# Optimization experiments

Measured on AMD Instinct MI355X. Metric: run time of the kernel, lower is better.

The kernel has to match this reference:

```python
import jax, jax.numpy as jnp
import numpy as np

N = 100_000   # nodes
E = 3_200_000 # edges (avg degree 32)
IN = 256      # input feature dim


def setup_inputs() -> dict:
    key = jax.random.key(0)
    ks = jax.random.split(key, 10)
    w = lambda k, s: (jax.random.normal(k, s, jnp.float32) * 0.02)
    return {
        "x": jax.random.normal(ks[0], (N, IN), jnp.float32),
        "edge_index": jax.random.randint(ks[1], (2, E), 0, N, dtype=jnp.int32),
        "edge_attr": jax.random.normal(ks[2], (E, 1), jnp.float32),
        # conv1: ExpGraphConv(IN, 64, 128)
        "W1a": w(ks[3], (IN, 64)), "b1a": jnp.zeros((64,), jnp.float32),
        "W1b": w(ks[4], (IN + 64, 128)), "b1b": jnp.zeros((128,), jnp.float32),
        # conv2: ExpGraphConv(128, 32->hidden 64? per ctor (128, 32, 64)): msg hidden 32... kept as repo: hidden=32? Using (128,64) msg, (192,64) out per faithful cat structure
        "W2a": w(ks[5], (128, 64)), "b2a": jnp.zeros((64,), jnp.float32),
        "W2b": w(ks[6], (128 + 64, 64)), "b2b": jnp.zeros((64,), jnp.float32),
        # head
        "Wl1": w(ks[7], (64, 32)), "bl1": jnp.zeros((32,), jnp.float32),
        "Wl2": w(ks[8], (32, 1)), "bl2": jnp.zeros((1,), jnp.float32),
    }


def _mean_aggr(h, src, dst, n):
    # gather messages from source nodes, scatter-mean into destination nodes
    s = jax.ops.segment_sum(h[src], dst, num_segments=n)          # [N, d]
    cnt = jax.ops.segment_sum(jnp.ones((src.shape[0],), h.dtype), dst, num_segments=n)
    return s / jnp.maximum(cnt, 1.0)[:, None]


def _exp_graph_conv(x, src, dst, Wa, ba, Wb, bb):
    # message MLP on source features, mean aggregation, then linear on [x || aggr]
    h = x @ Wa + ba                                               # [N, hidden]
    m = _mean_aggr(h, src, dst, x.shape[0])                       # [N, hidden]
    return jnp.concatenate([x, m], axis=1) @ Wb + bb              # [N, out]


def reference(x, edge_index, edge_attr, W1a, b1a, W1b, b1b, W2a, b2a, W2b, b2b, Wl1, bl1, Wl2, bl2):
    src, dst = edge_index[0], edge_index[1]
    x = jax.nn.relu(_exp_graph_conv(x, src, dst, W1a, b1a, W1b, b1b))
    x = jax.nn.relu(_exp_graph_conv(x, src, dst, W2a, b2a, W2b, b2b))
    x = jax.nn.relu(x @ Wl1 + bl1)
    return x @ Wl2 + bl2
```

## Files before the change

kernel.cpp:

```cpp
#include <hip/hip_runtime.h>
#include <type_traits>

#define IN_DIM 256
#define CAP 10240
#define EPB 4096

typedef _Float16 f16;
typedef _Float16 f16x8 __attribute__((ext_vector_type(8)));
typedef float f32x4 __attribute__((ext_vector_type(4)));


__global__ __launch_bounds__(256) void init_cur_k(int* __restrict__ bcur) {
    int i = blockIdx.x * 256 + threadIdx.x;
    if (i < 512) bcur[i] = i * CAP;
}

__global__ __launch_bounds__(256) void bucket_scatter_k(const int* __restrict__ srcp,
                                                        const int* __restrict__ dstp,
                                                        int* __restrict__ bcur,
                                                        unsigned* __restrict__ bedge, int E) {
    __shared__ int cnt[512], lstart[512], delta[512], fill[512];
    __shared__ int pfx[256];
    __shared__ unsigned spay[EPB];
    __shared__ unsigned char sbk[EPB];
    int tid = threadIdx.x;
    cnt[tid] = 0; cnt[tid + 256] = 0;
    fill[tid] = 0; fill[tid + 256] = 0;
    __syncthreads();
    size_t base = (size_t)blockIdx.x * EPB;
    int nloc = E - (int)base; if (nloc > EPB) nloc = EPB;
    int dreg[EPB / 256], sreg[EPB / 256];
#pragma unroll
    for (int j = 0; j < EPB / 256; j++) {
        int e = j * 256 + tid;
        if (e < nloc) {
            dreg[j] = dstp[base + e];
            sreg[j] = srcp[base + e];
            atomicAdd(&cnt[dreg[j] >> 8], 1);
        }
    }
    __syncthreads();
    int a0 = cnt[2 * tid], a1 = cnt[2 * tid + 1], s = a0 + a1;
    pfx[tid] = s;
    __syncthreads();
    for (int off = 1; off < 256; off <<= 1) {
        int t2 = (tid >= off) ? pfx[tid - off] : 0;
        __syncthreads();
        pfx[tid] += t2;
        __syncthreads();
    }
    int excl = pfx[tid] - s;
    lstart[2 * tid] = excl;
    lstart[2 * tid + 1] = excl + a0;
    int g0 = 0, g1 = 0;
    if (a0) g0 = atomicAdd(&bcur[2 * tid], a0);
    if (a1) g1 = atomicAdd(&bcur[2 * tid + 1], a1);
    delta[2 * tid] = g0 - excl;
    delta[2 * tid + 1] = g1 - (excl + a0);
    __syncthreads();
#pragma unroll
    for (int j = 0; j < EPB / 256; j++) {
        int e = j * 256 + tid;
        if (e < nloc) {
            int d = dreg[j], bk = d >> 8;
            int slot = lstart[bk] + atomicAdd(&fill[bk], 1);
            spay[slot] = (unsigned)sreg[j] | ((unsigned)(d & 255) << 17);
            sbk[slot] = (unsigned char)bk;
        }
    }
    __syncthreads();
    int mid = lstart[256];
#pragma unroll
    for (int j = 0; j < EPB / 256; j++) {
        int i = j * 256 + tid;
        if (i < nloc) {
            int bk = (int)sbk[i] | ((i >= mid) ? 256 : 0);
            int gp = i + delta[bk];
            if (gp < (bk + 1) * CAP)
                bedge[gp] = spay[i];
        }
    }
}

__global__ __launch_bounds__(256) void fine_sort_k(unsigned* __restrict__ bedge,
                                                   const int* __restrict__ bcur,
                                                   int2* __restrict__ ose, int Nn) {
    __shared__ int cnt[256], cur[256], pfx[256];
    __shared__ int sorted[CAP];
    int b = blockIdx.x, tid = threadIdx.x;
    int lo = b * CAP;
    int sz = bcur[b] - lo;
    if (sz > CAP) sz = CAP;
    cnt[tid] = 0;
    __syncthreads();
    for (int i = tid; i < sz; i += 256) atomicAdd(&cnt[bedge[lo + i] >> 17], 1);
    __syncthreads();
    int c = cnt[tid];
    pfx[tid] = c;
    __syncthreads();
    for (int off = 1; off < 256; off <<= 1) {
        int t2 = (tid >= off) ? pfx[tid - off] : 0;
        __syncthreads();
        pfx[tid] += t2;
        __syncthreads();
    }
    int excl = pfx[tid] - c;
    cur[tid] = excl;
    int node = b * 256 + tid;
    if (node < Nn) ose[node] = make_int2(lo + excl, lo + excl + c);
    __syncthreads();
    for (int i = tid; i < sz; i += 256) {
        unsigned v = bedge[lo + i];
        int slot = atomicAdd(&cur[v >> 17], 1);
        sorted[slot] = (int)(v & 0x1FFFFu);
    }
    __syncthreads();
    for (int i = tid; i < sz; i += 256) bedge[lo + i] = (unsigned)sorted[i];
}


__global__ __launch_bounds__(256) void castf16_k(const float* __restrict__ X,
                                                 f16* __restrict__ Y, int n4) {
    int i = blockIdx.x * 256 + threadIdx.x;
    if (i >= n4) return;
    float4 v = reinterpret_cast<const float4*>(X)[i];
    union { f16 h[4]; uint2 u; } p;
    p.h[0] = (f16)v.x; p.h[1] = (f16)v.y; p.h[2] = (f16)v.z; p.h[3] = (f16)v.w;
    reinterpret_cast<uint2*>(Y)[i] = p.u;
}

__global__ __launch_bounds__(256) void wcast_k(const float* __restrict__ W,
                                               f16* __restrict__ Wt, int K, int N) {
    int i = blockIdx.x * 256 + threadIdx.x;
    if (i >= N * K) return;
    int n = i / K, k = i - n * K;
    Wt[i] = (f16)W[(size_t)k * N + n];
}


__global__ __launch_bounds__(256) void aggr_k(const int2* __restrict__ ose,
                                              const int* __restrict__ ssrc,
                                              const f16* __restrict__ h,
                                              f16* __restrict__ m, int n) {
    int wave = (blockIdx.x * 256 + threadIdx.x) >> 6;
    int lane = threadIdx.x & 63;
    if (wave >= n) return;
    int2 se = ose[wave];
    int s0 = se.x, s1 = se.y;
    int half = lane >> 5;
    int l32 = lane & 31;
    const unsigned* h32 = reinterpret_cast<const unsigned*>(h);
    float ax = 0.f, ay = 0.f;
    for (int c = s0; c < s1; c += 64) {
        int cn = min(64, s1 - c);
        int myidx = (lane < cn) ? ssrc[c + lane] : 0;
        int t = 0;
        for (; t + 8 <= cn; t += 8) {
            int ia = __shfl(myidx, t + 0 + half);
            int ib = __shfl(myidx, t + 2 + half);
            int ic = __shfl(myidx, t + 4 + half);
            int id = __shfl(myidx, t + 6 + half);
            unsigned ua = h32[(size_t)ia * 32 + l32];
            unsigned ub = h32[(size_t)ib * 32 + l32];
            unsigned uc = h32[(size_t)ic * 32 + l32];
            unsigned ud = h32[(size_t)id * 32 + l32];
            union { unsigned u; f16 hh[2]; } qa, qb, qc, qd;
            qa.u = ua; qb.u = ub; qc.u = uc; qd.u = ud;
            ax += (float)qa.hh[0] + (float)qb.hh[0] + (float)qc.hh[0] + (float)qd.hh[0];
            ay += (float)qa.hh[1] + (float)qb.hh[1] + (float)qc.hh[1] + (float)qd.hh[1];
        }
        for (; t + 2 <= cn; t += 2) {
            int ia = __shfl(myidx, t + half);
            unsigned ua = h32[(size_t)ia * 32 + l32];
            union { unsigned u; f16 hh[2]; } qa; qa.u = ua;
            ax += (float)qa.hh[0];
            ay += (float)qa.hh[1];
        }
        if (t < cn) {
            int ia = __shfl(myidx, t);
            if (half == 0) {
                unsigned ua = h32[(size_t)ia * 32 + l32];
                union { unsigned u; f16 hh[2]; } qa; qa.u = ua;
                ax += (float)qa.hh[0];
                ay += (float)qa.hh[1];
            }
        }
    }
    ax += __shfl_xor(ax, 32);
    ay += __shfl_xor(ay, 32);
    if (half == 0) {
        float inv = 1.0f / fmaxf((float)(s1 - s0), 1.0f);
        union { unsigned u; f16 hh[2]; } q;
        q.hh[0] = (f16)(ax * inv);
        q.hh[1] = (f16)(ay * inv);
        reinterpret_cast<unsigned*>(m + (size_t)wave * 64)[l32] = q.u;
    }
}


template <int BN, bool OUT_F16>
__global__ __launch_bounds__(256) void gemm_mfma(const f16* __restrict__ A1, int K1,
                                                 const f16* __restrict__ A2, int K2,
                                                 const f16* __restrict__ Wt,
                                                 const float* __restrict__ bias,
                                                 void* __restrict__ Yv, int M, int relu) {
    constexpr int BM = 128, BK = 32;
    constexpr int WN = BN / 2;
    constexpr int NB = WN / 16;
    constexpr int SEGB = BN / 64;
    using T = typename std::conditional<OUT_F16, f16, float>::type;
    constexpr int EPS = BN + 8;
    constexpr int VECN = 16 / sizeof(T);
    constexpr int TPR = BN / VECN;
    constexpr size_t SM_AB = (size_t)BM * BK * 2 + (size_t)BN * BK * 2;
    constexpr size_t SM_EP = (size_t)BM * EPS * sizeof(T);
    constexpr size_t SM = SM_AB > SM_EP ? SM_AB : SM_EP;
    __shared__ __align__(16) char smem[SM];
    f16 (*As)[BK] = reinterpret_cast<f16(*)[BK]>(smem);
    f16 (*Bs)[BK] = reinterpret_cast<f16(*)[BK]>(smem + (size_t)BM * BK * 2);
    const int tid  = threadIdx.x;
    const int wave = tid >> 6;
    const int lane = tid & 63;
    const int wr   = wave >> 1;
    const int wc   = wave & 1;
    const int quad = lane >> 4;
    const int l16  = lane & 15;
    const int row0 = blockIdx.x * BM;
    const int Ktot = K1 + K2;

    f32x4 acc[4][NB];
#pragma unroll
    for (int i = 0; i < 4; i++)
#pragma unroll
        for (int j = 0; j < NB; j++) acc[i][j] = (f32x4)(0.f);

    const int ra = tid >> 2, sa = tid & 3;
    int rowA0 = row0 + ra;       if (rowA0 >= M) rowA0 = M - 1;
    int rowA1 = row0 + ra + 64;  if (rowA1 >= M) rowA1 = M - 1;

    uint4 aReg[2], bReg[SEGB];
    auto loadA = [&](int kk) {
        const f16* base; int stride, kloc;
        if (kk < K1) { base = A1; stride = K1; kloc = kk; }
        else         { base = A2; stride = K2; kloc = kk - K1; }
        aReg[0] = *reinterpret_cast<const uint4*>(base + (size_t)rowA0 * stride + kloc + sa * 8);
        aReg[1] = *reinterpret_cast<const uint4*>(base + (size_t)rowA1 * stride + kloc + sa * 8);
    };
    auto loadB = [&](int kk) {
#pragma unroll
        for (int i = 0; i < SEGB; i++) {
            int fid = tid + i * 256;
            int n = fid >> 2, s = fid & 3;
            bReg[i] = *reinterpret_cast<const uint4*>(Wt + (size_t)n * Ktot + kk + s * 8);
        }
    };

    loadA(0); loadB(0);
    for (int kk = 0; kk < Ktot; kk += BK) {
        reinterpret_cast<uint4*>(&As[0][0])[tid]       = aReg[0];
        reinterpret_cast<uint4*>(&As[0][0])[tid + 256] = aReg[1];
#pragma unroll
        for (int i = 0; i < SEGB; i++)
            reinterpret_cast<uint4*>(&Bs[0][0])[tid + i * 256] = bReg[i];
        __syncthreads();
        if (kk + BK < Ktot) { loadA(kk + BK); loadB(kk + BK); }
        f16x8 af[4], bf[NB];
#pragma unroll
        for (int rb = 0; rb < 4; rb++) {
            int row = wr * 64 + rb * 16 + l16;
            af[rb] = *reinterpret_cast<const f16x8*>(&As[row][quad * 8]);
        }
#pragma unroll
        for (int cb = 0; cb < NB; cb++) {
            int n = wc * WN + cb * 16 + l16;
            bf[cb] = *reinterpret_cast<const f16x8*>(&Bs[n][quad * 8]);
        }
#pragma unroll
        for (int rb = 0; rb < 4; rb++)
#pragma unroll
            for (int cb = 0; cb < NB; cb++)
                acc[rb][cb] = __builtin_amdgcn_mfma_f32_16x16x32_f16(af[rb], bf[cb], acc[rb][cb], 0, 0, 0);
        __syncthreads();
    }

    T* ep = reinterpret_cast<T*>(smem);
#pragma unroll
    for (int rb = 0; rb < 4; rb++) {
#pragma unroll
        for (int cb = 0; cb < NB; cb++) {
            int col = wc * WN + cb * 16 + l16;
            float bv = bias[col];
#pragma unroll
            for (int r = 0; r < 4; r++) {
                int lrow = wr * 64 + rb * 16 + quad * 4 + r;
                float v = acc[rb][cb][r] + bv;
                if (relu) v = fmaxf(v, 0.f);
                ep[(size_t)lrow * EPS + col] = (T)v;
            }
        }
    }
    __syncthreads();
#pragma unroll
    for (int p = 0; p < BM * TPR / 256; p++) {
        int fid = p * 256 + tid;
        int row = fid / TPR, c = fid % TPR;
        int grow = row0 + row;
        if (grow < M)
            *reinterpret_cast<uint4*>((T*)Yv + (size_t)grow * BN + c * VECN) =
                *reinterpret_cast<const uint4*>(ep + (size_t)row * EPS + c * VECN);
    }
}


__global__ __launch_bounds__(256) void head_k(const float* __restrict__ x2,
                                              const float* __restrict__ Wl1,
                                              const float* __restrict__ bl1,
                                              const float* __restrict__ Wl2,
                                              const float* __restrict__ bl2,
                                              float* __restrict__ out, int n) {
    __shared__ __align__(16) float w1[64 * 32];
    __shared__ float b1s[32];
    __shared__ float w2s[32];
    for (int t = threadIdx.x; t < 2048; t += 256) w1[t] = Wl1[t];
    if (threadIdx.x < 32) {
        b1s[threadIdx.x] = bl1[threadIdx.x];
        w2s[threadIdx.x] = Wl2[threadIdx.x];
    }
    __syncthreads();
    int i = blockIdx.x * 256 + threadIdx.x;
    if (i >= n) return;
    float v[64];
#pragma unroll
    for (int t = 0; t < 16; t++) {
        float4 q = *reinterpret_cast<const float4*>(x2 + (size_t)i * 64 + t * 4);
        v[t * 4 + 0] = q.x; v[t * 4 + 1] = q.y; v[t * 4 + 2] = q.z; v[t * 4 + 3] = q.w;
    }
    float hj[32];
#pragma unroll
    for (int j = 0; j < 32; j++) hj[j] = b1s[j];
    for (int k = 0; k < 64; k++) {
        float vk = v[k];
        const float4* wrow = reinterpret_cast<const float4*>(&w1[k * 32]);
#pragma unroll
        for (int j4 = 0; j4 < 8; j4++) {
            float4 wq = wrow[j4];
            hj[j4 * 4 + 0] += vk * wq.x;
            hj[j4 * 4 + 1] += vk * wq.y;
            hj[j4 * 4 + 2] += vk * wq.z;
            hj[j4 * 4 + 3] += vk * wq.w;
        }
    }
    float o = bl2[0];
#pragma unroll
    for (int j = 0; j < 32; j++) o += fmaxf(hj[j], 0.f) * w2s[j];
    out[i] = o;
}


extern "C" void kernel_launch(void* const* d_in, const int* in_sizes, int n_in,
                              void* d_out, int out_size, void* d_ws, size_t ws_size,
                              hipStream_t stream) {
    const float* x   = (const float*)d_in[0];
    const int*   ei  = (const int*)d_in[1];
    const float* W1a = (const float*)d_in[3];
    const float* b1a = (const float*)d_in[4];
    const float* W1b = (const float*)d_in[5];
    const float* b1b = (const float*)d_in[6];
    const float* W2a = (const float*)d_in[7];
    const float* b2a = (const float*)d_in[8];
    const float* W2b = (const float*)d_in[9];
    const float* b2b = (const float*)d_in[10];
    const float* Wl1 = (const float*)d_in[11];
    const float* bl1 = (const float*)d_in[12];
    const float* Wl2 = (const float*)d_in[13];
    const float* bl2 = (const float*)d_in[14];

    const int N = in_sizes[0] / IN_DIM;
    const int E = in_sizes[1] / 2;
    const int* srcp = ei;
    const int* dstp = ei + E;

    char* ws = (char*)d_ws;
    size_t off = 0;
    auto alloc = [&](size_t bytes) -> char* {
        char* p = ws + off;
        off = (off + bytes + 255) & ~(size_t)255;
        return p;
    };
    int NB2 = (N + 255) / 256;
    int*      bcur  = (int*)alloc(512 * 4);
    unsigned* bedge = (unsigned*)alloc((size_t)NB2 * CAP * 4);
    int2*     ose   = (int2*)alloc((size_t)N * 8);
    f16*      x16   = (f16*)alloc((size_t)N * IN_DIM * 2);
    f16*      hbuf  = (f16*)alloc((size_t)N * 64 * 2);
    f16*      mbuf  = (f16*)alloc((size_t)N * 64 * 2);
    f16*      x1    = (f16*)alloc((size_t)N * 128 * 2);
    float*    h2    = (float*)alloc((size_t)N * 64 * 4);
    f16*      Wt1a  = (f16*)alloc(256 * 64 * 2);
    f16*      Wt1b  = (f16*)alloc(320 * 128 * 2);
    f16*      Wt2a  = (f16*)alloc(128 * 64 * 2);
    f16*      Wt2b  = (f16*)alloc(192 * 64 * 2);
    (void)ws_size;

    init_cur_k<<<2, 256, 0, stream>>>(bcur);
    int ebk = (E + EPB - 1) / EPB;
    bucket_scatter_k<<<ebk, 256, 0, stream>>>(srcp, dstp, bcur, bedge, E);
    fine_sort_k<<<NB2, 256, 0, stream>>>(bedge, bcur, ose, N);

    int n4 = N * IN_DIM / 4;
    castf16_k<<<(n4 + 255) / 256, 256, 0, stream>>>(x, x16, n4);
    wcast_k<<<(256 * 64 + 255) / 256, 256, 0, stream>>>(W1a, Wt1a, 256, 64);
    wcast_k<<<(320 * 128 + 255) / 256, 256, 0, stream>>>(W1b, Wt1b, 320, 128);
    wcast_k<<<(128 * 64 + 255) / 256, 256, 0, stream>>>(W2a, Wt2a, 128, 64);
    wcast_k<<<(192 * 64 + 255) / 256, 256, 0, stream>>>(W2b, Wt2b, 192, 64);

    int mb = (N + 127) / 128;
    int ab = (N * 64 + 255) / 256;

    gemm_mfma<64, true><<<mb, 256, 0, stream>>>(x16, IN_DIM, nullptr, 0, Wt1a, b1a, hbuf, N, 0);
    aggr_k<<<ab, 256, 0, stream>>>(ose, (const int*)bedge, hbuf, mbuf, N);
    gemm_mfma<128, true><<<mb, 256, 0, stream>>>(x16, IN_DIM, mbuf, 64, Wt1b, b1b, x1, N, 1);

    gemm_mfma<64, true><<<mb, 256, 0, stream>>>(x1, 128, nullptr, 0, Wt2a, b2a, hbuf, N, 0);
    aggr_k<<<ab, 256, 0, stream>>>(ose, (const int*)bedge, hbuf, mbuf, N);
    gemm_mfma<64, false><<<mb, 256, 0, stream>>>(x1, 128, mbuf, 64, Wt2b, b2b, h2, N, 1);

    head_k<<<(N + 255) / 256, 256, 0, stream>>>(h2, Wl1, bl1, Wl2, bl2, (float*)d_out, N);
}
```

Baseline: 515.2 us.

## Halve GEMM row tile, add nontemporal loads/stores, store h2 as f16

The GEMM row tile drops from 128 to 64, which launches twice as many blocks with fewer accumulators each. The cast kernel and the GEMM A-operand loads and selected outputs now use nontemporal loads and stores to reduce cache pollution. The layer-2 output h2 is stored as f16 rather than fp32 and read as f16 in the head, halving that traffic at some precision cost. Smaller tiles mean more weight (B) reloads per row processed.

```diff
diff --git a/kernel.cpp b/kernel.cpp
--- a/kernel.cpp
+++ b/kernel.cpp
@@ -8,6 +8,8 @@
 typedef _Float16 f16;
 typedef _Float16 f16x8 __attribute__((ext_vector_type(8)));
 typedef float f32x4 __attribute__((ext_vector_type(4)));
+typedef unsigned u32x4 __attribute__((ext_vector_type(4)));
+typedef unsigned u32x2 __attribute__((ext_vector_type(2)));
 
 
 __global__ __launch_bounds__(256) void init_cur_k(int* __restrict__ bcur) {
@@ -123,10 +125,10 @@
                                                  f16* __restrict__ Y, int n4) {
     int i = blockIdx.x * 256 + threadIdx.x;
     if (i >= n4) return;
-    float4 v = reinterpret_cast<const float4*>(X)[i];
-    union { f16 h[4]; uint2 u; } p;
+    f32x4 v = __builtin_nontemporal_load(reinterpret_cast<const f32x4*>(X) + i);
+    union { f16 h[4]; u32x2 u; } p;
     p.h[0] = (f16)v.x; p.h[1] = (f16)v.y; p.h[2] = (f16)v.z; p.h[3] = (f16)v.w;
-    reinterpret_cast<uint2*>(Y)[i] = p.u;
+    __builtin_nontemporal_store(p.u, reinterpret_cast<u32x2*>(Y) + i);
 }
 
 __global__ __launch_bounds__(256) void wcast_k(const float* __restrict__ W,
@@ -203,8 +205,9 @@
                                                  const f16* __restrict__ A2, int K2,
                                                  const f16* __restrict__ Wt,
                                                  const float* __restrict__ bias,
-                                                 void* __restrict__ Yv, int M, int relu) {
-    constexpr int BM = 128, BK = 32;
+                                                 void* __restrict__ Yv, int M, int relu,
+                                                 int stream_out) {
+    constexpr int BM = 64, BK = 32;
     constexpr int WN = BN / 2;
     constexpr int NB = WN / 16;
     constexpr int SEGB = BN / 64;
@@ -228,46 +231,44 @@
     const int row0 = blockIdx.x * BM;
     const int Ktot = K1 + K2;
 
-    f32x4 acc[4][NB];
-#pragma unroll
-    for (int i = 0; i < 4; i++)
+    f32x4 acc[2][NB];
+#pragma unroll
+    for (int i = 0; i < 2; i++)
 #pragma unroll
         for (int j = 0; j < NB; j++) acc[i][j] = (f32x4)(0.f);
 
     const int ra = tid >> 2, sa = tid & 3;
-    int rowA0 = row0 + ra;       if (rowA0 >= M) rowA0 = M - 1;
-    int rowA1 = row0 + ra + 64;  if (rowA1 >= M) rowA1 = M - 1;
-
-    uint4 aReg[2], bReg[SEGB];
+    int rowA = row0 + ra;  if (rowA >= M) rowA = M - 1;
+
+    u32x4 aReg, bReg[SEGB];
     auto loadA = [&](int kk) {
         const f16* base; int stride, kloc;
         if (kk < K1) { base = A1; stride = K1; kloc = kk; }
         else         { base = A2; stride = K2; kloc = kk - K1; }
-        aReg[0] = *reinterpret_cast<const uint4*>(base + (size_t)rowA0 * stride + kloc + sa * 8);
-        aReg[1] = *reinterpret_cast<const uint4*>(base + (size_t)rowA1 * stride + kloc + sa * 8);
+        aReg = __builtin_nontemporal_load(
+            reinterpret_cast<const u32x4*>(base + (size_t)rowA * stride + kloc + sa * 8));
     };
     auto loadB = [&](int kk) {
 #pragma unroll
         for (int i = 0; i < SEGB; i++) {
             int fid = tid + i * 256;
             int n = fid >> 2, s = fid & 3;
-            bReg[i] = *reinterpret_cast<const uint4*>(Wt + (size_t)n * Ktot + kk + s * 8);
+            bReg[i] = *reinterpret_cast<const u32x4*>(Wt + (size_t)n * Ktot + kk + s * 8);
         }
     };
 
     loadA(0); loadB(0);
     for (int kk = 0; kk < Ktot; kk += BK) {
-        reinterpret_cast<uint4*>(&As[0][0])[tid]       = aReg[0];
-        reinterpret_cast<uint4*>(&As[0][0])[tid + 256] = aReg[1];
+        reinterpret_cast<u32x4*>(&As[0][0])[tid] = aReg;
 #pragma unroll
         for (int i = 0; i < SEGB; i++)
-            reinterpret_cast<uint4*>(&Bs[0][0])[tid + i * 256] = bReg[i];
+            reinterpret_cast<u32x4*>(&Bs[0][0])[tid + i * 256] = bReg[i];
         __syncthreads();
         if (kk + BK < Ktot) { loadA(kk + BK); loadB(kk + BK); }
-        f16x8 af[4], bf[NB];
-#pragma unroll
-        for (int rb = 0; rb < 4; rb++) {
-            int row = wr * 64 + rb * 16 + l16;
+        f16x8 af[2], bf[NB];
+#pragma unroll
+        for (int rb = 0; rb < 2; rb++) {
+            int row = wr * 32 + rb * 16 + l16;
             af[rb] = *reinterpret_cast<const f16x8*>(&As[row][quad * 8]);
         }
 #pragma unroll
@@ -276,7 +277,7 @@
             bf[cb] = *reinterpret_cast<const f16x8*>(&Bs[n][quad * 8]);
         }
 #pragma unroll
-        for (int rb = 0; rb < 4; rb++)
+        for (int rb = 0; rb < 2; rb++)
 #pragma unroll
             for (int cb = 0; cb < NB; cb++)
                 acc[rb][cb] = __builtin_amdgcn_mfma_f32_16x16x32_f16(af[rb], bf[cb], acc[rb][cb], 0, 0, 0);
@@ -285,14 +286,14 @@
 
     T* ep = reinterpret_cast<T*>(smem);
 #pragma unroll
-    for (int rb = 0; rb < 4; rb++) {
+    for (int rb = 0; rb < 2; rb++) {
 #pragma unroll
         for (int cb = 0; cb < NB; cb++) {
             int col = wc * WN + cb * 16 + l16;
             float bv = bias[col];
 #pragma unroll
             for (int r = 0; r < 4; r++) {
-                int lrow = wr * 64 + rb * 16 + quad * 4 + r;
+                int lrow = wr * 32 + rb * 16 + quad * 4 + r;
                 float v = acc[rb][cb][r] + bv;
                 if (relu) v = fmaxf(v, 0.f);
                 ep[(size_t)lrow * EPS + col] = (T)v;
@@ -305,14 +306,17 @@
         int fid = p * 256 + tid;
         int row = fid / TPR, c = fid % TPR;
         int grow = row0 + row;
-        if (grow < M)
-            *reinterpret_cast<uint4*>((T*)Yv + (size_t)grow * BN + c * VECN) =
-                *reinterpret_cast<const uint4*>(ep + (size_t)row * EPS + c * VECN);
-    }
-}
-
-
-__global__ __launch_bounds__(256) void head_k(const float* __restrict__ x2,
+        if (grow < M) {
+            u32x4 val = *reinterpret_cast<const u32x4*>(ep + (size_t)row * EPS + c * VECN);
+            u32x4* dst = reinterpret_cast<u32x4*>((T*)Yv + (size_t)grow * BN + c * VECN);
+            if (stream_out) __builtin_nontemporal_store(val, dst);
+            else            *dst = val;
+        }
+    }
+}
+
+
+__global__ __launch_bounds__(256) void head_k(const f16* __restrict__ x2,
                                               const float* __restrict__ Wl1,
                                               const float* __restrict__ bl1,
                                               const float* __restrict__ Wl2,
@@ -330,10 +334,12 @@
     int i = blockIdx.x * 256 + threadIdx.x;
     if (i >= n) return;
     float v[64];
-#pragma unroll
-    for (int t = 0; t < 16; t++) {
-        float4 q = *reinterpret_cast<const float4*>(x2 + (size_t)i * 64 + t * 4);
-        v[t * 4 + 0] = q.x; v[t * 4 + 1] = q.y; v[t * 4 + 2] = q.z; v[t * 4 + 3] = q.w;
+    const f16x8* xr = reinterpret_cast<const f16x8*>(x2 + (size_t)i * 64);
+#pragma unroll
+    for (int t = 0; t < 8; t++) {
+        f16x8 q = xr[t];
+#pragma unroll
+        for (int j = 0; j < 8; j++) v[t * 8 + j] = (float)q[j];
     }
     float hj[32];
 #pragma unroll
@@ -395,7 +401,7 @@
     f16*      hbuf  = (f16*)alloc((size_t)N * 64 * 2);
     f16*      mbuf  = (f16*)alloc((size_t)N * 64 * 2);
     f16*      x1    = (f16*)alloc((size_t)N * 128 * 2);
-    float*    h2    = (float*)alloc((size_t)N * 64 * 4);
+    f16*      h2    = (f16*)alloc((size_t)N * 64 * 2);
     f16*      Wt1a  = (f16*)alloc(256 * 64 * 2);
     f16*      Wt1b  = (f16*)alloc(320 * 128 * 2);
     f16*      Wt2a  = (f16*)alloc(128 * 64 * 2);
@@ -414,16 +420,16 @@
     wcast_k<<<(128 * 64 + 255) / 256, 256, 0, stream>>>(W2a, Wt2a, 128, 64);
     wcast_k<<<(192 * 64 + 255) / 256, 256, 0, stream>>>(W2b, Wt2b, 192, 64);
 
-    int mb = (N + 127) / 128;
+    int mb = (N + 63) / 64;
     int ab = (N * 64 + 255) / 256;
 
-    gemm_mfma<64, true><<<mb, 256, 0, stream>>>(x16, IN_DIM, nullptr, 0, Wt1a, b1a, hbuf, N, 0);
+    gemm_mfma<64, true><<<mb, 256, 0, stream>>>(x16, IN_DIM, nullptr, 0, Wt1a, b1a, hbuf, N, 0, 0);
     aggr_k<<<ab, 256, 0, stream>>>(ose, (const int*)bedge, hbuf, mbuf, N);
-    gemm_mfma<128, true><<<mb, 256, 0, stream>>>(x16, IN_DIM, mbuf, 64, Wt1b, b1b, x1, N, 1);
-
-    gemm_mfma<64, true><<<mb, 256, 0, stream>>>(x1, 128, nullptr, 0, Wt2a, b2a, hbuf, N, 0);
+    gemm_mfma<128, true><<<mb, 256, 0, stream>>>(x16, IN_DIM, mbuf, 64, Wt1b, b1b, x1, N, 1, 1);
+
+    gemm_mfma<64, true><<<mb, 256, 0, stream>>>(x1, 128, nullptr, 0, Wt2a, b2a, hbuf, N, 0, 0);
     aggr_k<<<ab, 256, 0, stream>>>(ose, (const int*)bedge, hbuf, mbuf, N);
-    gemm_mfma<64, false><<<mb, 256, 0, stream>>>(x1, 128, mbuf, 64, Wt2b, b2b, h2, N, 1);
+    gemm_mfma<64, true><<<mb, 256, 0, stream>>>(x1, 128, mbuf, 64, Wt2b, b2b, h2, N, 1, 1);
 
     head_k<<<(N + 255) / 256, 256, 0, stream>>>(h2, Wl1, bl1, Wl2, bl2, (float*)d_out, N);
 }
```

Measured after the change: 475.8 us. 1.08x faster.
